# Performance work log

Measured on AMD Instinct MI355X. Metric: run time of the kernel, lower is better.

Reference implementation:

```python
import jax, jax.numpy as jnp
import numpy as np

T, D, L, H = 512, 256, 256, 512  # tokens, embed dim, lstm dims, hidden units


def _lstm(x, W, U, b):
    """Keras-style LSTM over x [T, Din] -> hidden states [T, L].
    Gate order i, f, g(cell), o; sigmoid recurrent activations, tanh cell."""
    Ldim = U.shape[0]

    def step(carry, xt):
        h, c = carry
        z = xt @ W + h @ U + b  # [4L]
        i, f, g, o = jnp.split(z, 4)
        i = jax.nn.sigmoid(i)
        f = jax.nn.sigmoid(f)
        g = jnp.tanh(g)
        o = jax.nn.sigmoid(o)
        c = f * c + i * g
        h = o * jnp.tanh(c)
        return (h, c), h

    h0 = jnp.zeros((Ldim,), x.dtype)
    _, hs = jax.lax.scan(step, (h0, h0), x)
    return hs


def setup_inputs() -> dict:
    key = jax.random.key(0)
    ks = jax.random.split(key, 16)

    def p(k, shape):
        # Glorot-like small init
        fan = shape[0] + shape[-1]
        return jax.random.normal(k, shape, jnp.float32) * np.float32(np.sqrt(2.0 / fan))

    return {
        "embeddings": jax.random.normal(ks[0], (1, T, D), jnp.float32),
        "W_f1": p(ks[1], (D, 4 * L)), "U_f1": p(ks[2], (L, 4 * L)), "b_f1": jnp.zeros((4 * L,), jnp.float32),
        "W_b1": p(ks[3], (D, 4 * L)), "U_b1": p(ks[4], (L, 4 * L)), "b_b1": jnp.zeros((4 * L,), jnp.float32),
        "W_f2": p(ks[5], (2 * L, 4 * L)), "U_f2": p(ks[6], (L, 4 * L)), "b_f2": jnp.zeros((4 * L,), jnp.float32),
        "W_b2": p(ks[7], (2 * L, 4 * L)), "U_b2": p(ks[8], (L, 4 * L)), "b_b2": jnp.zeros((4 * L,), jnp.float32),
        "FOH": p(ks[9], (2 * L, H)),
        "FOM": p(ks[10], (2 * L, H)),
        "hidBias": p(ks[11], (1, H)),
        "outLayer": p(ks[12], (H, 1)),
        "outBias": p(ks[13], (1, 1)),
    }


def reference(embeddings, W_f1, U_f1, b_f1, W_b1, U_b1, b_b1,
              W_f2, U_f2, b_f2, W_b2, U_b2, b_b2,
              FOH, FOM, hidBias, outLayer, outBias):
    x = embeddings[0]  # [T, D]
    # --- FirstBiLSTMModule ---
    rf1 = _lstm(x, W_f1, U_f1, b_f1)            # forward LSTM over sequence
    rb1 = _lstm(x[::-1], W_b1, U_b1, b_b1)      # backward LSTM over reversed sequence
    # concatenate_layers: pair forward step i with backward step T-1-i
    v = jnp.concatenate([rf1, rb1[::-1]], axis=-1)  # [T, 2L]
    # --- NextBiLSTMModule ---
    rf2 = _lstm(v, W_f2, U_f2, b_f2)
    rb2 = _lstm(v[::-1], W_b2, U_b2, b_b2)
    hcat = jnp.concatenate([rf2, rb2[::-1]], axis=-1)  # [T, 2L] per-token concat
    # --- ConcatHeadModule.__evaluate (hidden2_units == 0 path) ---
    headfov = hcat @ FOH  # [T, H]
    modfov = hcat @ FOM   # [T, H]
    # pairwise: activation(headfov_i + modfov_j + hidBias) @ outLayer + outBias
    act = jnp.tanh(headfov[:, None, :] + modfov[None, :, :] + hidBias[0])  # [T, T, H]
    scores = jnp.einsum('ijh,ho->ij', act, outLayer) + outBias[0, 0]       # [T, T]
    return scores
```

## Files before the change

### kernel.cpp

```cpp
#include <hip/hip_runtime.h>
#include <hip/hip_bf16.h>


typedef _Float16 h2v __attribute__((ext_vector_type(2)));
typedef unsigned int u32x32 __attribute__((ext_vector_type(32)));

#define BC(x) __builtin_bit_cast(h2v, (x))

__device__ __forceinline__ float fdot2f(h2v a, h2v b, float c) {
#if __has_builtin(__builtin_amdgcn_fdot2)
    return __builtin_amdgcn_fdot2(a, b, c, false);
#else
    return c + (float)a[0] * (float)b[0] + (float)a[1] * (float)b[1];
#endif
}

__global__ __launch_bounds__(256) void prep_u(const float* __restrict__ U,
                                              unsigned int* __restrict__ Uf) {
    int idx = blockIdx.x * 256 + threadIdx.x;
    int k2 = idx >> 10, col = idx & 1023;
    union { _Float16 h[2]; unsigned int u; } p;
    p.h[0] = (_Float16)U[(2 * k2) * 1024 + col];
    p.h[1] = (_Float16)U[(2 * k2 + 1) * 1024 + col];
    Uf[idx] = p.u;
}

__global__ __launch_bounds__(256) void gemm_bias(const float* __restrict__ A,
                                                 const float* __restrict__ B,
                                                 const float* __restrict__ bias,
                                                 float* __restrict__ C,
                                                 int M, int N, int K, int revA) {
    __shared__ float sA[16][65];
    __shared__ float sB[16][65];
    int tid = threadIdx.x;
    int bm = blockIdx.y * 64, bn = blockIdx.x * 64;
    int tx = tid & 15, ty = tid >> 4;
    float acc[4][4] = {};
    for (int k0 = 0; k0 < K; k0 += 16) {
#pragma unroll
        for (int l = 0; l < 4; l++) {
            int flat = tid + 256 * l;
            int ml = flat >> 4, kk = flat & 15;
            int row = bm + ml;
            if (revA) row = M - 1 - row;
            sA[kk][ml] = A[row * K + k0 + kk];
        }
#pragma unroll
        for (int l = 0; l < 4; l++) {
            int flat = tid + 256 * l;
            int kk = flat >> 6, nl = flat & 63;
            sB[kk][nl] = B[(k0 + kk) * N + bn + nl];
        }
        __syncthreads();
#pragma unroll
        for (int kk = 0; kk < 16; kk++) {
            float a[4], b[4];
#pragma unroll
            for (int i = 0; i < 4; i++) a[i] = sA[kk][ty + 16 * i];
#pragma unroll
            for (int j = 0; j < 4; j++) b[j] = sB[kk][tx + 16 * j];
#pragma unroll
            for (int i = 0; i < 4; i++)
#pragma unroll
                for (int j = 0; j < 4; j++) acc[i][j] += a[i] * b[j];
        }
        __syncthreads();
    }
#pragma unroll
    for (int i = 0; i < 4; i++) {
        int r = bm + ty + 16 * i;
#pragma unroll
        for (int j = 0; j < 4; j++) {
            int cidx = bn + tx + 16 * j;
            float bv = bias ? bias[cidx] : 0.f;
            C[r * N + cidx] = acc[i][j] + bv;
        }
    }
}

#define KLDS 32
#define KREG 96

#define UR0(r) ((r) < 32 ? u0a[(r) & 31] : (r) < 64 ? u0b[(r) & 31] : u0c[(r) & 31])
#define UR1(r) ((r) < 32 ? u1a[(r) & 31] : (r) < 64 ? u1b[(r) & 31] : u1c[(r) & 31])

__global__ __attribute__((amdgpu_flat_work_group_size(512, 512),
                          amdgpu_waves_per_eu(2, 2)))
void lstm_two(
        const unsigned int* __restrict__ Ua, const unsigned int* __restrict__ Ub,
        const float* __restrict__ Pa, const float* __restrict__ Pb,
        float* __restrict__ Oa, float* __restrict__ Ob) {
    const unsigned int* U = blockIdx.x ? Ub : Ua;
    const float* P = blockIdx.x ? Pb : Pa;
    float* O = blockIdx.x ? Ob : Oa;

    __shared__ unsigned int sU[KLDS * 1024];
    __shared__ __align__(16) _Float16 sH[256];
    __shared__ float sZ[1024];

    int t = threadIdx.x;

    for (int i = t; i < KLDS * 1024; i += 512) sU[i] = U[i];

    u32x32 u0a, u0b, u0c, u1a, u1b, u1c;
#pragma unroll
    for (int r = 0; r < 32; r++) {
        uint2 w;
        w = *(const uint2*)&U[(KLDS + r) * 1024 + 2 * t];
        u0a[r] = w.x; u1a[r] = w.y;
        w = *(const uint2*)&U[(KLDS + 32 + r) * 1024 + 2 * t];
        u0b[r] = w.x; u1b[r] = w.y;
        w = *(const uint2*)&U[(KLDS + 64 + r) * 1024 + 2 * t];
        u0c[r] = w.x; u1c[r] = w.y;
    }

    float c = 0.f;
    if (t < 256) sH[t] = (_Float16)0.f;
    __syncthreads();

    const uint4* hp4 = (const uint4*)sH;
    float2 pc = *(const float2*)(P + 2 * t);
    for (int step = 0; step < 512; step++) {
        float2 pn = pc;
        if (step < 511) pn = *(const float2*)(P + (step + 1) * 1024 + 2 * t);
        float acc0 = pc.x, acc1 = pc.y;

#pragma unroll
        for (int cch = 0; cch < 8; cch++) {
            uint4 hc = hp4[cch];
            const unsigned int* su = &sU[(4 * cch) * 1024 + 2 * t];
            uint2 w;
            w = *(const uint2*)(su);
            acc0 = fdot2f(BC(hc.x), BC(w.x), acc0);
            acc1 = fdot2f(BC(hc.x), BC(w.y), acc1);
            w = *(const uint2*)(su + 1024);
            acc0 = fdot2f(BC(hc.y), BC(w.x), acc0);
            acc1 = fdot2f(BC(hc.y), BC(w.y), acc1);
            w = *(const uint2*)(su + 2048);
            acc0 = fdot2f(BC(hc.z), BC(w.x), acc0);
            acc1 = fdot2f(BC(hc.z), BC(w.y), acc1);
            w = *(const uint2*)(su + 3072);
            acc0 = fdot2f(BC(hc.w), BC(w.x), acc0);
            acc1 = fdot2f(BC(hc.w), BC(w.y), acc1);
        }
#pragma unroll
        for (int cch = 0; cch < 24; cch++) {
            uint4 hc = hp4[8 + cch];
            const int r0 = 4 * cch;
            acc0 = fdot2f(BC(hc.x), BC(UR0(r0 + 0)), acc0);
            acc1 = fdot2f(BC(hc.x), BC(UR1(r0 + 0)), acc1);
            acc0 = fdot2f(BC(hc.y), BC(UR0(r0 + 1)), acc0);
            acc1 = fdot2f(BC(hc.y), BC(UR1(r0 + 1)), acc1);
            acc0 = fdot2f(BC(hc.z), BC(UR0(r0 + 2)), acc0);
            acc1 = fdot2f(BC(hc.z), BC(UR1(r0 + 2)), acc1);
            acc0 = fdot2f(BC(hc.w), BC(UR0(r0 + 3)), acc0);
            acc1 = fdot2f(BC(hc.w), BC(UR1(r0 + 3)), acc1);
        }
        ((float2*)sZ)[t] = make_float2(acc0, acc1);
        __syncthreads();
        if (t < 256) {
            float zi = sZ[t], zf = sZ[256 + t], zg = sZ[512 + t], zo = sZ[768 + t];
            float ig = 1.f / (1.f + __expf(-zi));
            float fg = 1.f / (1.f + __expf(-zf));
            float gg = 1.f - 2.f / (1.f + __expf(2.f * zg));
            float og = 1.f / (1.f + __expf(-zo));
            c = fg * c + ig * gg;
            float h = og * (1.f - 2.f / (1.f + __expf(2.f * c)));
            O[step * 256 + t] = h;
            sH[t] = (_Float16)h;
        }
        __syncthreads();
        pc = pn;
    }
}

__global__ __launch_bounds__(256) void concat_k(const float* __restrict__ F,
                                                const float* __restrict__ Bk,
                                                float* __restrict__ V) {
    int idx = blockIdx.x * 256 + threadIdx.x;
    int t = idx >> 9, d = idx & 511;
    V[idx] = (d < 256) ? F[t * 256 + d] : Bk[(511 - t) * 256 + d - 256];
}

__global__ __launch_bounds__(256) void head_kernel(const float* __restrict__ HF,
                                                   const float* __restrict__ MF,
                                                   const float* __restrict__ w,
                                                   const float* __restrict__ outb,
                                                   float* __restrict__ S) {
    int i = blockIdx.x;
    __shared__ float sHF[512], sW[512];
    int tid = threadIdx.x;
    sHF[tid] = HF[i * 512 + tid];
    sHF[tid + 256] = HF[i * 512 + 256 + tid];
    sW[tid] = w[tid];
    sW[tid + 256] = w[tid + 256];
    __syncthreads();
    int lane = tid & 63, wv = tid >> 6;
    float ob = outb[0];
    for (int j = wv; j < 512; j += 4) {
        const float* mf = MF + j * 512;
        float acc = 0.f;
#pragma unroll
        for (int r = 0; r < 8; r++) {
            int h = lane + 64 * r;
            float x = sHF[h] + mf[h];
            acc += sW[h] * (1.f - 2.f / (1.f + __expf(2.f * x)));
        }
#pragma unroll
        for (int off = 32; off; off >>= 1) acc += __shfl_down(acc, off);
        if (lane == 0) S[i * 512 + j] = acc + ob;
    }
}

extern "C" void kernel_launch(void* const* d_in, const int* in_sizes, int n_in,
                              void* d_out, int out_size, void* d_ws, size_t ws_size,
                              hipStream_t stream) {
    const float* emb      = (const float*)d_in[0];
    const float* W_f1     = (const float*)d_in[1];
    const float* U_f1     = (const float*)d_in[2];
    const float* b_f1     = (const float*)d_in[3];
    const float* W_b1     = (const float*)d_in[4];
    const float* U_b1     = (const float*)d_in[5];
    const float* b_b1     = (const float*)d_in[6];
    const float* W_f2     = (const float*)d_in[7];
    const float* U_f2     = (const float*)d_in[8];
    const float* b_f2     = (const float*)d_in[9];
    const float* W_b2     = (const float*)d_in[10];
    const float* U_b2     = (const float*)d_in[11];
    const float* b_b2     = (const float*)d_in[12];
    const float* FOH      = (const float*)d_in[13];
    const float* FOM      = (const float*)d_in[14];
    const float* hidBias  = (const float*)d_in[15];
    const float* outLayer = (const float*)d_in[16];
    const float* outBias  = (const float*)d_in[17];
    float* out = (float*)d_out;

    unsigned int* uf = (unsigned int*)d_ws;
    unsigned int* uf_f1 = uf;
    unsigned int* uf_b1 = uf + 131072;
    unsigned int* uf_f2 = uf + 262144;
    unsigned int* uf_b2 = uf + 393216;
    float* f = (float*)d_ws + 524288;
    float* P1f = f;
    float* P1b = f + 524288;
    float* P2f = f + 1048576;
    float* P2b = f + 1572864;
    float* rf1 = f + 2097152;
    float* rb1 = f + 2228224;
    float* rf2 = f + 2359296;
    float* rb2 = f + 2490368;
    float* v    = f + 2621440;
    float* hcat = f + 2883584;
    float* HFb  = f + 3145728;
    float* MFb  = f + 3407872;

    prep_u<<<512, 256, 0, stream>>>(U_f1, uf_f1);
    prep_u<<<512, 256, 0, stream>>>(U_b1, uf_b1);
    prep_u<<<512, 256, 0, stream>>>(U_f2, uf_f2);
    prep_u<<<512, 256, 0, stream>>>(U_b2, uf_b2);

    dim3 g1(1024 / 64, 512 / 64);
    gemm_bias<<<g1, 256, 0, stream>>>(emb, W_f1, b_f1, P1f, 512, 1024, 256, 0);
    gemm_bias<<<g1, 256, 0, stream>>>(emb, W_b1, b_b1, P1b, 512, 1024, 256, 1);

    lstm_two<<<2, 512, 0, stream>>>(uf_f1, uf_b1, P1f, P1b, rf1, rb1);

    concat_k<<<1024, 256, 0, stream>>>(rf1, rb1, v);

    gemm_bias<<<g1, 256, 0, stream>>>(v, W_f2, b_f2, P2f, 512, 1024, 512, 0);
    gemm_bias<<<g1, 256, 0, stream>>>(v, W_b2, b_b2, P2b, 512, 1024, 512, 1);

    lstm_two<<<2, 512, 0, stream>>>(uf_f2, uf_b2, P2f, P2b, rf2, rb2);

    concat_k<<<1024, 256, 0, stream>>>(rf2, rb2, hcat);

    dim3 g2(512 / 64, 512 / 64);
    gemm_bias<<<g2, 256, 0, stream>>>(hcat, FOH, hidBias, HFb, 512, 512, 512, 0);
    gemm_bias<<<g2, 256, 0, stream>>>(hcat, FOM, nullptr, MFb, 512, 512, 512, 0);

    head_kernel<<<512, 256, 0, stream>>>(HFb, MFb, outLayer, outBias, out);
}
```

Measured before the change: 2.748 ms.

## Use 1024 threads per LSTM block, one gate column per thread

The recurrent LSTM kernel now runs 1024 threads per block instead of 512, so each thread computes a single gate column rather than two. Each thread holds half as many register-resident U rows (96 rows in twelve 8-wide vectors, pinned with an empty asm). Per-step dot-product latency per thread is halved, and the two partial accumulators are summed before the gate activations. The cost is more waves per CU, so the 512-thread barrier-heavy serial loop now synchronizes 16 waves, and register pressure must fit the 4-waves-per-EU limit.

Measured after the change: 2.825 ms. +2.8%, slower.

```diff
diff --git a/kernel.cpp b/kernel.cpp
--- a/kernel.cpp
+++ b/kernel.cpp
@@ -3,7 +3,7 @@
 
 
 typedef _Float16 h2v __attribute__((ext_vector_type(2)));
-typedef unsigned int u32x32 __attribute__((ext_vector_type(32)));
+typedef unsigned int u32x8 __attribute__((ext_vector_type(8)));
 
 #define BC(x) __builtin_bit_cast(h2v, (x))
 
@@ -81,11 +81,20 @@
 #define KLDS 32
 #define KREG 96
 
-#define UR0(r) ((r) < 32 ? u0a[(r) & 31] : (r) < 64 ? u0b[(r) & 31] : u0c[(r) & 31])
-#define UR1(r) ((r) < 32 ? u1a[(r) & 31] : (r) < 64 ? u1b[(r) & 31] : u1c[(r) & 31])
-
-__global__ __attribute__((amdgpu_flat_work_group_size(512, 512),
-                          amdgpu_waves_per_eu(2, 2)))
+#define UA(r) ((r) < 8 ? q0[(r) & 7] : (r) < 16 ? q1[(r) & 7] : (r) < 24 ? q2[(r) & 7] : \
+               (r) < 32 ? q3[(r) & 7] : (r) < 40 ? q4[(r) & 7] : (r) < 48 ? q5[(r) & 7] : \
+               (r) < 56 ? q6[(r) & 7] : (r) < 64 ? q7[(r) & 7] : (r) < 72 ? q8[(r) & 7] : \
+               (r) < 80 ? q9[(r) & 7] : (r) < 88 ? q10[(r) & 7] : q11[(r) & 7])
+
+#define LOADQ(qi, va)                                                   \
+    do {                                                                \
+        _Pragma("unroll") for (int j = 0; j < 8; j++) {                 \
+            va[j] = U[(KLDS + 8 * (qi) + j) * 1024 + t];                \
+        }                                                               \
+    } while (0)
+
+__global__ __attribute__((amdgpu_flat_work_group_size(1024, 1024),
+                          amdgpu_waves_per_eu(4, 4)))
 void lstm_two(
         const unsigned int* __restrict__ Ua, const unsigned int* __restrict__ Ub,
         const float* __restrict__ Pa, const float* __restrict__ Pb,
@@ -100,63 +109,47 @@
 
     int t = threadIdx.x;
 
-    for (int i = t; i < KLDS * 1024; i += 512) sU[i] = U[i];
-
-    u32x32 u0a, u0b, u0c, u1a, u1b, u1c;
-#pragma unroll
-    for (int r = 0; r < 32; r++) {
-        uint2 w;
-        w = *(const uint2*)&U[(KLDS + r) * 1024 + 2 * t];
-        u0a[r] = w.x; u1a[r] = w.y;
-        w = *(const uint2*)&U[(KLDS + 32 + r) * 1024 + 2 * t];
-        u0b[r] = w.x; u1b[r] = w.y;
-        w = *(const uint2*)&U[(KLDS + 64 + r) * 1024 + 2 * t];
-        u0c[r] = w.x; u1c[r] = w.y;
-    }
+    for (int i = t; i < KLDS * 1024; i += 1024) sU[i] = U[i];
+
+    u32x8 q0, q1, q2, q3, q4, q5, q6, q7, q8, q9, q10, q11;
+    LOADQ(0, q0);   LOADQ(1, q1);   LOADQ(2, q2);   LOADQ(3, q3);
+    LOADQ(4, q4);   LOADQ(5, q5);   LOADQ(6, q6);   LOADQ(7, q7);
+    LOADQ(8, q8);   LOADQ(9, q9);   LOADQ(10, q10); LOADQ(11, q11);
+
+    asm volatile(""
+                 : "+v"(q0), "+v"(q1), "+v"(q2), "+v"(q3), "+v"(q4), "+v"(q5),
+                   "+v"(q6), "+v"(q7), "+v"(q8), "+v"(q9), "+v"(q10), "+v"(q11));
 
     float c = 0.f;
     if (t < 256) sH[t] = (_Float16)0.f;
     __syncthreads();
 
     const uint4* hp4 = (const uint4*)sH;
-    float2 pc = *(const float2*)(P + 2 * t);
+    float pc = P[t];
     for (int step = 0; step < 512; step++) {
-        float2 pn = pc;
-        if (step < 511) pn = *(const float2*)(P + (step + 1) * 1024 + 2 * t);
-        float acc0 = pc.x, acc1 = pc.y;
+        float pn = pc;
+        if (step < 511) pn = P[(step + 1) * 1024 + t];
+        float acc0 = pc, acc1 = 0.f;
 
 #pragma unroll
         for (int cch = 0; cch < 8; cch++) {
             uint4 hc = hp4[cch];
-            const unsigned int* su = &sU[(4 * cch) * 1024 + 2 * t];
-            uint2 w;
-            w = *(const uint2*)(su);
-            acc0 = fdot2f(BC(hc.x), BC(w.x), acc0);
-            acc1 = fdot2f(BC(hc.x), BC(w.y), acc1);
-            w = *(const uint2*)(su + 1024);
-            acc0 = fdot2f(BC(hc.y), BC(w.x), acc0);
-            acc1 = fdot2f(BC(hc.y), BC(w.y), acc1);
-            w = *(const uint2*)(su + 2048);
-            acc0 = fdot2f(BC(hc.z), BC(w.x), acc0);
-            acc1 = fdot2f(BC(hc.z), BC(w.y), acc1);
-            w = *(const uint2*)(su + 3072);
-            acc0 = fdot2f(BC(hc.w), BC(w.x), acc0);
-            acc1 = fdot2f(BC(hc.w), BC(w.y), acc1);
+            const unsigned int* su = &sU[(4 * cch) * 1024 + t];
+            acc0 = fdot2f(BC(hc.x), BC(su[0]), acc0);
+            acc1 = fdot2f(BC(hc.y), BC(su[1024]), acc1);
+            acc0 = fdot2f(BC(hc.z), BC(su[2048]), acc0);
+            acc1 = fdot2f(BC(hc.w), BC(su[3072]), acc1);
         }
 #pragma unroll
         for (int cch = 0; cch < 24; cch++) {
             uint4 hc = hp4[8 + cch];
             const int r0 = 4 * cch;
-            acc0 = fdot2f(BC(hc.x), BC(UR0(r0 + 0)), acc0);
-            acc1 = fdot2f(BC(hc.x), BC(UR1(r0 + 0)), acc1);
-            acc0 = fdot2f(BC(hc.y), BC(UR0(r0 + 1)), acc0);
-            acc1 = fdot2f(BC(hc.y), BC(UR1(r0 + 1)), acc1);
-            acc0 = fdot2f(BC(hc.z), BC(UR0(r0 + 2)), acc0);
-            acc1 = fdot2f(BC(hc.z), BC(UR1(r0 + 2)), acc1);
-            acc0 = fdot2f(BC(hc.w), BC(UR0(r0 + 3)), acc0);
-            acc1 = fdot2f(BC(hc.w), BC(UR1(r0 + 3)), acc1);
-        }
-        ((float2*)sZ)[t] = make_float2(acc0, acc1);
+            acc0 = fdot2f(BC(hc.x), BC(UA(r0 + 0)), acc0);
+            acc1 = fdot2f(BC(hc.y), BC(UA(r0 + 1)), acc1);
+            acc0 = fdot2f(BC(hc.z), BC(UA(r0 + 2)), acc0);
+            acc1 = fdot2f(BC(hc.w), BC(UA(r0 + 3)), acc1);
+        }
+        sZ[t] = acc0 + acc1;
         __syncthreads();
         if (t < 256) {
             float zi = sZ[t], zf = sZ[256 + t], zg = sZ[512 + t], zo = sZ[768 + t];
@@ -263,14 +256,14 @@
     gemm_bias<<<g1, 256, 0, stream>>>(emb, W_f1, b_f1, P1f, 512, 1024, 256, 0);
     gemm_bias<<<g1, 256, 0, stream>>>(emb, W_b1, b_b1, P1b, 512, 1024, 256, 1);
 
-    lstm_two<<<2, 512, 0, stream>>>(uf_f1, uf_b1, P1f, P1b, rf1, rb1);
+    lstm_two<<<2, 1024, 0, stream>>>(uf_f1, uf_b1, P1f, P1b, rf1, rb1);
 
     concat_k<<<1024, 256, 0, stream>>>(rf1, rb1, v);
 
     gemm_bias<<<g1, 256, 0, stream>>>(v, W_f2, b_f2, P2f, 512, 1024, 512, 0);
     gemm_bias<<<g1, 256, 0, stream>>>(v, W_b2, b_b2, P2b, 512, 1024, 512, 1);
 
-    lstm_two<<<2, 512, 0, stream>>>(uf_f2, uf_b2, P2f, P2b, rf2, rb2);
+    lstm_two<<<2, 1024, 0, stream>>>(uf_f2, uf_b2, P2f, P2b, rf2, rb2);
 
     concat_k<<<1024, 256, 0, stream>>>(rf2, rb2, hcat);
 
```
